# Kernel tuning notes

Measured on AMD Instinct MI355X. Metric: run time of the kernel, lower is better.

Reference implementation:

```python
import jax, jax.numpy as jnp
import numpy as np
from jax import lax

BETA = 0.5        # Sinkhron beta
N_ITER = 20       # got_iteration
THRESH = 0.1      # P > 0.1 threshold
NL_I = 5          # apply_non_linearity(..., 'elu', i=5)
EPS = 1e-9


def setup_inputs() -> dict:
    key = jax.random.key(0)
    k1, k2 = jax.random.split(key)
    B, N, D = 128, 512, 128
    h = jax.random.normal(k1, (B, N, D), dtype=jnp.float32)
    W0 = jnp.ones((D,), dtype=jnp.float32)
    W1 = jnp.ones((D,), dtype=jnp.float32)
    lengths = jax.random.randint(k2, (B,), 0, N, dtype=jnp.int32)
    return {"h": h, "W0": W0, "W1": W1, "lengths": lengths}


def _forward(h, W0, W1, lengths):
    B, N, D = h.shape
    lengths = jnp.maximum(lengths, 1)
    mask = (jnp.arange(N)[None, :] < lengths[:, None])          # [B, N] bool
    mf = mask.astype(h.dtype)
    mask2 = mf[:, :, None] * mf[:, None, :]                      # [B, N, N]

    # internal_forward: Diag layers with relu between (mlp_act='relu')
    h = h * W0
    h = jax.nn.relu(h)
    h = h * W1

    # cost_matrix_batch_torch: cosine similarity, add identity diag, mask
    hn = h / (jnp.linalg.norm(h, axis=-1, keepdims=True) + 1e-12)
    sim = jnp.einsum('bnd,bmd->bnm', hn, hn)                     # [B, N, N]
    sim = sim + jnp.eye(N, dtype=h.dtype)                        # add_eye_diag
    sim = sim * mask2
    cost = (1.0 - sim) * mask2

    # Sinkhorn with uniform marginals on valid nodes, fixed iterations
    n = lengths.astype(h.dtype)
    mu = mf / n[:, None]                                         # [B, N]
    K = jnp.exp(-cost / BETA) * mask2                            # [B, N, N]

    def body(carry, _):
        u, v = carry
        u = mu / (jnp.einsum('bnm,bm->bn', K, v) + EPS) * mf
        v = mu / (jnp.einsum('bnm,bn->bm', K, u) + EPS) * mf
        return (u, v), None

    (u, v), _ = lax.scan(body, (mf, mf), None, length=N_ITER)
    P = u[:, :, None] * K * v[:, None, :]                        # transport plan

    # P.detach(); scale by number of nodes per graph; threshold
    P = lax.stop_gradient(P)
    P = n[:, None, None] * P
    A = (P > THRESH).astype(h.dtype)
    similarity = A * sim
    # apply_non_linearity 'elu': elu(x*i - i) + 1
    out = jax.nn.elu(similarity * NL_I - NL_I) + 1.0
    return out


def reference(h, W0, W1, lengths):
    return _forward(h, W0, W1, lengths)
```

## Files before the change

kernel.cpp:

```cpp
#include <hip/hip_runtime.h>

#define BB 128
#define NN 512
#define DD 128
#define SLOT_STRIDE 544

__global__ __launch_bounds__(256) void hn_kernel(const float* __restrict__ h,
                                                 const float* __restrict__ W0,
                                                 const float* __restrict__ W1,
                                                 float* __restrict__ hn) {
    int wave = (int)((blockIdx.x * blockDim.x + threadIdx.x) >> 6);
    int lane = threadIdx.x & 63;
    const float2* h2 = (const float2*)(h + (size_t)wave * DD);
    float2 w0 = ((const float2*)W0)[lane];
    float2 w1 = ((const float2*)W1)[lane];
    float2 x = h2[lane];
    float p0 = fmaxf(x.x * w0.x, 0.0f) * w1.x;
    float p1 = fmaxf(x.y * w0.y, 0.0f) * w1.y;
    float ss = p0 * p0 + p1 * p1;
#pragma unroll
    for (int m = 32; m; m >>= 1) ss += __shfl_xor(ss, m);
    float inv = 1.0f / (sqrtf(ss) + 1e-12f);
    float2 o;
    o.x = p0 * inv;
    o.y = p1 * inv;
    ((float2*)(hn + (size_t)wave * DD))[lane] = o;
}

#define KC 32
__global__ __launch_bounds__(256) void sim_kernel(const float* __restrict__ hn,
                                                  const int* __restrict__ lengths,
                                                  float* __restrict__ K) {
    __shared__ float As[KC][132];
    __shared__ float Bs[KC][132];
    __shared__ int pre[BB + 1];
    int tid = threadIdx.x;
    if (tid == 0) {
        int acc = 0;
        for (int b = 0; b < BB; b++) {
            pre[b] = acc;
            int len = max(lengths[b], 1);
            int nt = (len + 127) >> 7;
            acc += nt * nt;
        }
        pre[BB] = acc;
    }
    __syncthreads();
    int total = pre[BB];

    int lr = tid >> 3;
    int lk = (tid & 7) << 2;
    int tx = tid & 15, ty = tid >> 4;

    for (int t = blockIdx.x; t < total; t += gridDim.x) {
        int lo = 0, hi = BB;
        while (lo + 1 < hi) {
            int mid = (lo + hi) >> 1;
            if (pre[mid] <= t) lo = mid; else hi = mid;
        }
        int b = lo;
        int local = t - pre[b];
        int len = max(lengths[b], 1);
        int nt = (len + 127) >> 7;
        int ti = local / nt;
        int tj = local - ti * nt;
        int r0 = ti << 7, c0 = tj << 7;
        const float* base = hn + (size_t)b * NN * DD;
        float acc[8][8] = {};

        for (int kc = 0; kc < DD; kc += KC) {
#pragma unroll
            for (int rr = 0; rr < 128; rr += 32) {
                float4 a = *(const float4*)(base + (size_t)(r0 + lr + rr) * DD + kc + lk);
                As[lk + 0][lr + rr] = a.x; As[lk + 1][lr + rr] = a.y;
                As[lk + 2][lr + rr] = a.z; As[lk + 3][lr + rr] = a.w;
                float4 bb = *(const float4*)(base + (size_t)(c0 + lr + rr) * DD + kc + lk);
                Bs[lk + 0][lr + rr] = bb.x; Bs[lk + 1][lr + rr] = bb.y;
                Bs[lk + 2][lr + rr] = bb.z; Bs[lk + 3][lr + rr] = bb.w;
            }
            __syncthreads();
#pragma unroll
            for (int kk = 0; kk < KC; kk++) {
                float4 a0 = *(const float4*)&As[kk][ty * 8];
                float4 a1 = *(const float4*)&As[kk][ty * 8 + 4];
                float4 b0 = *(const float4*)&Bs[kk][tx * 4];
                float4 b1 = *(const float4*)&Bs[kk][64 + tx * 4];
                float ar[8] = {a0.x, a0.y, a0.z, a0.w, a1.x, a1.y, a1.z, a1.w};
                float bc[8] = {b0.x, b0.y, b0.z, b0.w, b1.x, b1.y, b1.z, b1.w};
#pragma unroll
                for (int r = 0; r < 8; r++)
#pragma unroll
                    for (int c = 0; c < 8; c++)
                        acc[r][c] = fmaf(ar[r], bc[c], acc[r][c]);
            }
            __syncthreads();
        }
        float* out = K + (size_t)b * NN * NN;
#pragma unroll
        for (int r = 0; r < 8; r++) {
            int i = r0 + ty * 8 + r;
            if (i >= len) continue;
#pragma unroll
            for (int cg = 0; cg < 2; cg++) {
                int j0 = c0 + cg * 64 + tx * 4;
                if (j0 >= len) continue;
                float vv[4];
#pragma unroll
                for (int c = 0; c < 4; c++) {
                    float s = acc[r][cg * 4 + c] + ((i == j0 + c) ? 1.0f : 0.0f);
                    vv[c] = expf(2.0f * s - 2.0f);
                }
                float4 o;
                o.x = vv[0]; o.y = vv[1]; o.z = vv[2]; o.w = vv[3];
                *(float4*)(out + (size_t)i * NN + j0) = o;
            }
        }
    }
}

__device__ __forceinline__ float dot8(float4 A, float4 B, float4 x0, float4 x1) {
    float d = fmaf(A.x, x0.x, fmaf(A.y, x0.y, fmaf(A.z, x0.z, A.w * x0.w)));
    return fmaf(B.x, x1.x, fmaf(B.y, x1.y, fmaf(B.z, x1.z, fmaf(B.w, x1.w, d))));
}

__global__ __launch_bounds__(512, 4) void coop_sink(const float* __restrict__ K,
                                                    float* __restrict__ u_buf,
                                                    float* __restrict__ v_buf,
                                                    const int* __restrict__ lengths,
                                                    float* __restrict__ slots) {
    __shared__ float xb[NN];
    __shared__ float pv[8 * NN];
    __shared__ int Sh[BB], Pre[BB];

    int g = blockIdx.x;
    int tid = threadIdx.x;

    if (tid == 0) {
        int need[BB]; int ssum = 0;
        for (int m = 0; m < BB; m++) {
            int L = max(lengths[m], 1);
            need[m] = (L + 79) / 80;
            ssum += need[m];
        }
        while (ssum > 512) {
            int best = 0, bv = need[0];
            for (int m = 1; m < BB; m++)
                if (need[m] > bv) { bv = need[m]; best = m; }
            need[best]--; ssum--;
        }
        int acc = 0;
        for (int m = 0; m < BB; m++) { Pre[m] = acc; Sh[m] = need[m]; acc += need[m]; }
    }
    __syncthreads();

    int m = -1;
    for (int mm = 0; mm < BB; mm++)
        if (g >= Pre[mm] && g < Pre[mm] + Sh[mm]) { m = mm; break; }
    if (m < 0) return;
    int b = m;
    int jbase = Pre[m];
    int q = g - jbase;
    int S = Sh[m];

    int len = max(lengths[b], 1);
    int len4 = (len + 3) & ~3;
    int rpq = (len + S - 1) / S;
    int r_lo = q * rpq;
    int nrows = min(len - r_lo, rpq);
    if (nrows < 0) nrows = 0;
    float inv_n = 1.0f / (float)len;

    int w = tid >> 6, l = tid & 63;
    int c0 = 4 * l, c1 = 256 + 4 * l;
    bool a0 = c0 < len4, a1 = c1 < len4;
    const float* Kb = K + (size_t)b * NN * NN;

    xb[tid] = (tid < len) ? 1.0f : 0.0f;

    float4 kA0 = {0,0,0,0}, kA1 = {0,0,0,0}, kA2 = {0,0,0,0}, kA3 = {0,0,0,0};
    float4 kA4 = {0,0,0,0}, kA5 = {0,0,0,0}, kA6 = {0,0,0,0}, kA7 = {0,0,0,0};
    float4 kA8 = {0,0,0,0}, kA9 = {0,0,0,0};
    float4 kB0 = {0,0,0,0}, kB1 = {0,0,0,0}, kB2 = {0,0,0,0}, kB3 = {0,0,0,0};
    float4 kB4 = {0,0,0,0}, kB5 = {0,0,0,0}, kB6 = {0,0,0,0}, kB7 = {0,0,0,0};
    float4 kB8 = {0,0,0,0}, kB9 = {0,0,0,0};
#define FILL_ROW(o)                                                          \
    {                                                                        \
        int i_ = w + 8 * o;                                                  \
        if (i_ < nrows) {                                                    \
            const float* g0_ = Kb + (size_t)(r_lo + i_) * NN;                \
            if (a0) kA##o = *(const float4*)(g0_ + c0);                      \
            if (a1) kB##o = *(const float4*)(g0_ + c1);                      \
        }                                                                    \
    }
    FILL_ROW(0) FILL_ROW(1) FILL_ROW(2) FILL_ROW(3) FILL_ROW(4)
    FILL_ROW(5) FILL_ROW(6) FILL_ROW(7) FILL_ROW(8) FILL_ROW(9)
#undef FILL_ROW

    __syncthreads();

    for (int t = 0; t < 20; t++) {
        float4 xv0 = *(const float4*)(xb + c0);
        float4 xv1 = *(const float4*)(xb + c1);
        float4 pa = {0, 0, 0, 0}, pb = {0, 0, 0, 0};

        float d0 = dot8(kA0, kB0, xv0, xv1);
        float d1 = dot8(kA1, kB1, xv0, xv1);
        float d2 = dot8(kA2, kB2, xv0, xv1);
        float d3 = dot8(kA3, kB3, xv0, xv1);
        float d4 = dot8(kA4, kB4, xv0, xv1);
        float d5 = dot8(kA5, kB5, xv0, xv1);
        float d6 = dot8(kA6, kB6, xv0, xv1);
        float d7 = dot8(kA7, kB7, xv0, xv1);
        float d8 = dot8(kA8, kB8, xv0, xv1);
        float d9 = dot8(kA9, kB9, xv0, xv1);
#pragma unroll
        for (int mm = 32; mm; mm >>= 1) {
            d0 += __shfl_xor(d0, mm); d1 += __shfl_xor(d1, mm);
            d2 += __shfl_xor(d2, mm); d3 += __shfl_xor(d3, mm);
            d4 += __shfl_xor(d4, mm); d5 += __shfl_xor(d5, mm);
            d6 += __shfl_xor(d6, mm); d7 += __shfl_xor(d7, mm);
            d8 += __shfl_xor(d8, mm); d9 += __shfl_xor(d9, mm);
        }
        float u0 = inv_n / (d0 + 1e-9f), u1 = inv_n / (d1 + 1e-9f);
        float u2 = inv_n / (d2 + 1e-9f), u3 = inv_n / (d3 + 1e-9f);
        float u4 = inv_n / (d4 + 1e-9f), u5 = inv_n / (d5 + 1e-9f);
        float u6 = inv_n / (d6 + 1e-9f), u7 = inv_n / (d7 + 1e-9f);
        float u8 = inv_n / (d8 + 1e-9f), u9 = inv_n / (d9 + 1e-9f);
#define ACC_ROW(o, uo)                                                       \
    pa.x = fmaf(kA##o.x, uo, pa.x); pa.y = fmaf(kA##o.y, uo, pa.y);          \
    pa.z = fmaf(kA##o.z, uo, pa.z); pa.w = fmaf(kA##o.w, uo, pa.w);          \
    pb.x = fmaf(kB##o.x, uo, pb.x); pb.y = fmaf(kB##o.y, uo, pb.y);          \
    pb.z = fmaf(kB##o.z, uo, pb.z); pb.w = fmaf(kB##o.w, uo, pb.w);
        ACC_ROW(0, u0) ACC_ROW(1, u1) ACC_ROW(2, u2) ACC_ROW(3, u3)
        ACC_ROW(4, u4) ACC_ROW(5, u5) ACC_ROW(6, u6) ACC_ROW(7, u7)
        ACC_ROW(8, u8) ACC_ROW(9, u9)
#undef ACC_ROW
        if (t == 19 && l == 0) {
            float* ub = u_buf + (size_t)b * NN + r_lo + w;
            if (w + 0 < nrows) ub[0] = u0;
            if (w + 8 < nrows) ub[8] = u1;
            if (w + 16 < nrows) ub[16] = u2;
            if (w + 24 < nrows) ub[24] = u3;
            if (w + 32 < nrows) ub[32] = u4;
            if (w + 40 < nrows) ub[40] = u5;
            if (w + 48 < nrows) ub[48] = u6;
            if (w + 56 < nrows) ub[56] = u7;
            if (w + 64 < nrows) ub[64] = u8;
            if (w + 72 < nrows) ub[72] = u9;
        }

        for (int i = 80 + w; i < nrows; i += 8) {
            const float* g0 = Kb + (size_t)(r_lo + i) * NN;
            float4 A = {0, 0, 0, 0}, B = {0, 0, 0, 0};
            if (a0) A = *(const float4*)(g0 + c0);
            if (a1) B = *(const float4*)(g0 + c1);
            float d = dot8(A, B, xv0, xv1);
#pragma unroll
            for (int mm = 32; mm; mm >>= 1) d += __shfl_xor(d, mm);
            float uu = inv_n / (d + 1e-9f);
            pa.x = fmaf(A.x, uu, pa.x); pa.y = fmaf(A.y, uu, pa.y);
            pa.z = fmaf(A.z, uu, pa.z); pa.w = fmaf(A.w, uu, pa.w);
            pb.x = fmaf(B.x, uu, pb.x); pb.y = fmaf(B.y, uu, pb.y);
            pb.z = fmaf(B.z, uu, pb.z); pb.w = fmaf(B.w, uu, pb.w);
            if (t == 19 && l == 0) u_buf[(size_t)b * NN + r_lo + i] = uu;
        }

        *(float4*)(pv + w * NN + c0) = pa;
        *(float4*)(pv + w * NN + c1) = pb;
        __syncthreads();
        float* slotp = slots + ((size_t)(t & 1) * 512 + g) * SLOT_STRIDE;
        int c = tid;
        float s0 = pv[c] + pv[NN + c] + pv[2 * NN + c] + pv[3 * NN + c] +
                   pv[4 * NN + c] + pv[5 * NN + c] + pv[6 * NN + c] + pv[7 * NN + c];
        __hip_atomic_store(slotp + c, s0, __ATOMIC_RELAXED, __HIP_MEMORY_SCOPE_AGENT);
        asm volatile("s_waitcnt vmcnt(0)" ::: "memory");
        __syncthreads();
        if (tid == 0)
            __hip_atomic_store((int*)(slotp + 512), t + 1, __ATOMIC_RELAXED,
                               __HIP_MEMORY_SCOPE_AGENT);
        if (tid < S && tid != q) {
            const int* tagp = (const int*)(slots +
                ((size_t)(t & 1) * 512 + (size_t)(jbase + tid)) * SLOT_STRIDE + 512);
            while (__hip_atomic_load(tagp, __ATOMIC_RELAXED, __HIP_MEMORY_SCOPE_AGENT) != t + 1)
                __builtin_amdgcn_s_sleep(1);
        }
        __syncthreads();

        const float* sbase = slots + ((size_t)(t & 1) * 512) * SLOT_STRIDE;
        float t0 = s0;
        for (int s = 1; s < S; s++) {
            int k = q + s; if (k >= S) k -= S;
            t0 += __hip_atomic_load(sbase + (size_t)(jbase + k) * SLOT_STRIDE + c,
                                    __ATOMIC_RELAXED, __HIP_MEMORY_SCOPE_AGENT);
        }
        float v0 = (c < len) ? (inv_n / (t0 + 1e-9f)) : 0.0f;
        if (t < 19) {
            xb[c] = v0;
        } else if (c >= r_lo && c < r_lo + nrows) {
            v_buf[(size_t)b * NN + c] = v0;
        }
        __syncthreads();
    }
}

__global__ __launch_bounds__(256) void epi_kernel(float* __restrict__ io,
                                                  const float* __restrict__ u,
                                                  const float* __restrict__ v,
                                                  const int* __restrict__ lengths) {
    const float E5 = 0.006737946999085467f;
    size_t idx = (size_t)blockIdx.x * 256 + threadIdx.x;
    int b = (int)(idx >> 16);
    int r = (int)(idx >> 7) & (NN - 1);
    int c4 = ((int)idx & 127) << 2;
    int len = max(lengths[b], 1);
    float4 o;
    if (r >= len || c4 >= len) {
        o.x = E5; o.y = E5; o.z = E5; o.w = E5;
        ((float4*)io)[idx] = o;
        return;
    }
    float4 k = ((float4*)io)[idx];
    float ui = u[(size_t)b * NN + r];
    float4 vv = *(const float4*)(v + (size_t)b * NN + c4);
    float t = (float)len * ui;
    float kv[4] = {k.x, k.y, k.z, k.w};
    float vj[4] = {vv.x, vv.y, vv.z, vv.w};
    float ov[4];
#pragma unroll
    for (int c = 0; c < 4; c++) {
        float Kc = kv[c];
        float P = t * Kc * vj[c];
        bool valid = (c4 + c) < len;
        if (valid && P > 0.1f) {
            float x = 2.5f * logf(Kc);
            ov[c] = (x > 0.0f) ? (x + 1.0f) : expf(x);
        } else {
            ov[c] = E5;
        }
    }
    o.x = ov[0]; o.y = ov[1]; o.z = ov[2]; o.w = ov[3];
    ((float4*)io)[idx] = o;
}

extern "C" void kernel_launch(void* const* d_in, const int* in_sizes, int n_in,
                              void* d_out, int out_size, void* d_ws, size_t ws_size,
                              hipStream_t stream) {
    const float* h = (const float*)d_in[0];
    const float* W0 = (const float*)d_in[1];
    const float* W1 = (const float*)d_in[2];
    const int* lengths = (const int*)d_in[3];
    float* K = (float*)d_out;

    char* ws = (char*)d_ws;
    float* hn = (float*)ws;
    size_t off = (size_t)BB * NN * DD * 4;
    float* u = (float*)(ws + off);     off += (size_t)BB * NN * 4;
    float* v = (float*)(ws + off);     off += (size_t)BB * NN * 4;
    float* slots = (float*)(ws + off); off += (size_t)2 * 512 * SLOT_STRIDE * 4;

    hn_kernel<<<BB * NN / 4, 256, 0, stream>>>(h, W0, W1, hn);
    sim_kernel<<<1024, 256, 0, stream>>>(hn, lengths, K);

    coop_sink<<<512, 512, 0, stream>>>(K, u, v, lengths, slots);

    epi_kernel<<<(unsigned)((size_t)BB * NN * NN / 4 / 256), 256, 0, stream>>>(K, u, v, lengths);
}
```

Baseline: 393.9 us.

## Cache 176 K rows per block in registers and halve the Sinkhorn grid

Each workgroup now keeps up to 176 rows of K in registers instead of 80, so a graph is split across fewer blocks. The persistent Sinkhorn grid drops from 512 to 256 blocks, and launch bounds allow 2 blocks per CU instead of 4. This cuts cross-block slot exchange and spin-wait synchronisation per iteration, and skips the slot publishing when a graph fits in one block. The cost is much higher register pressure (44 float4 per thread), which risks spills and lower occupancy.

```diff
diff --git a/kernel.cpp b/kernel.cpp
--- a/kernel.cpp
+++ b/kernel.cpp
@@ -123,7 +123,10 @@
     return fmaf(B.x, x1.x, fmaf(B.y, x1.y, fmaf(B.z, x1.z, fmaf(B.w, x1.w, d))));
 }
 
-__global__ __launch_bounds__(512, 4) void coop_sink(const float* __restrict__ K,
+#define ROWS22(X) X(0) X(1) X(2) X(3) X(4) X(5) X(6) X(7) X(8) X(9) X(10) \
+    X(11) X(12) X(13) X(14) X(15) X(16) X(17) X(18) X(19) X(20) X(21)
+
+__global__ __launch_bounds__(512, 2) void coop_sink(const float* __restrict__ K,
                                                     float* __restrict__ u_buf,
                                                     float* __restrict__ v_buf,
                                                     const int* __restrict__ lengths,
@@ -139,10 +142,10 @@
         int need[BB]; int ssum = 0;
         for (int m = 0; m < BB; m++) {
             int L = max(lengths[m], 1);
-            need[m] = (L + 79) / 80;
+            need[m] = (L + 175) / 176;
             ssum += need[m];
         }
-        while (ssum > 512) {
+        while (ssum > 256) {
             int best = 0, bv = need[0];
             for (int m = 1; m < BB; m++)
                 if (need[m] > bv) { bv = need[m]; best = m; }
@@ -177,23 +180,19 @@
 
     xb[tid] = (tid < len) ? 1.0f : 0.0f;
 
-    float4 kA0 = {0,0,0,0}, kA1 = {0,0,0,0}, kA2 = {0,0,0,0}, kA3 = {0,0,0,0};
-    float4 kA4 = {0,0,0,0}, kA5 = {0,0,0,0}, kA6 = {0,0,0,0}, kA7 = {0,0,0,0};
-    float4 kA8 = {0,0,0,0}, kA9 = {0,0,0,0};
-    float4 kB0 = {0,0,0,0}, kB1 = {0,0,0,0}, kB2 = {0,0,0,0}, kB3 = {0,0,0,0};
-    float4 kB4 = {0,0,0,0}, kB5 = {0,0,0,0}, kB6 = {0,0,0,0}, kB7 = {0,0,0,0};
-    float4 kB8 = {0,0,0,0}, kB9 = {0,0,0,0};
+#define DECL(o) float4 kA##o = {0,0,0,0}, kB##o = {0,0,0,0};
+    ROWS22(DECL)
+#undef DECL
 #define FILL_ROW(o)                                                          \
     {                                                                        \
-        int i_ = w + 8 * o;                                                  \
+        int i_ = w + 8 * (o);                                                \
         if (i_ < nrows) {                                                    \
             const float* g0_ = Kb + (size_t)(r_lo + i_) * NN;                \
             if (a0) kA##o = *(const float4*)(g0_ + c0);                      \
             if (a1) kB##o = *(const float4*)(g0_ + c1);                      \
         }                                                                    \
     }
-    FILL_ROW(0) FILL_ROW(1) FILL_ROW(2) FILL_ROW(3) FILL_ROW(4)
-    FILL_ROW(5) FILL_ROW(6) FILL_ROW(7) FILL_ROW(8) FILL_ROW(9)
+    ROWS22(FILL_ROW)
 #undef FILL_ROW
 
     __syncthreads();
@@ -203,53 +202,33 @@
         float4 xv1 = *(const float4*)(xb + c1);
         float4 pa = {0, 0, 0, 0}, pb = {0, 0, 0, 0};
 
-        float d0 = dot8(kA0, kB0, xv0, xv1);
-        float d1 = dot8(kA1, kB1, xv0, xv1);
-        float d2 = dot8(kA2, kB2, xv0, xv1);
-        float d3 = dot8(kA3, kB3, xv0, xv1);
-        float d4 = dot8(kA4, kB4, xv0, xv1);
-        float d5 = dot8(kA5, kB5, xv0, xv1);
-        float d6 = dot8(kA6, kB6, xv0, xv1);
-        float d7 = dot8(kA7, kB7, xv0, xv1);
-        float d8 = dot8(kA8, kB8, xv0, xv1);
-        float d9 = dot8(kA9, kB9, xv0, xv1);
+#define DOT(o) float d##o = dot8(kA##o, kB##o, xv0, xv1);
+        ROWS22(DOT)
+#undef DOT
 #pragma unroll
         for (int mm = 32; mm; mm >>= 1) {
-            d0 += __shfl_xor(d0, mm); d1 += __shfl_xor(d1, mm);
-            d2 += __shfl_xor(d2, mm); d3 += __shfl_xor(d3, mm);
-            d4 += __shfl_xor(d4, mm); d5 += __shfl_xor(d5, mm);
-            d6 += __shfl_xor(d6, mm); d7 += __shfl_xor(d7, mm);
-            d8 += __shfl_xor(d8, mm); d9 += __shfl_xor(d9, mm);
-        }
-        float u0 = inv_n / (d0 + 1e-9f), u1 = inv_n / (d1 + 1e-9f);
-        float u2 = inv_n / (d2 + 1e-9f), u3 = inv_n / (d3 + 1e-9f);
-        float u4 = inv_n / (d4 + 1e-9f), u5 = inv_n / (d5 + 1e-9f);
-        float u6 = inv_n / (d6 + 1e-9f), u7 = inv_n / (d7 + 1e-9f);
-        float u8 = inv_n / (d8 + 1e-9f), u9 = inv_n / (d9 + 1e-9f);
-#define ACC_ROW(o, uo)                                                       \
-    pa.x = fmaf(kA##o.x, uo, pa.x); pa.y = fmaf(kA##o.y, uo, pa.y);          \
-    pa.z = fmaf(kA##o.z, uo, pa.z); pa.w = fmaf(kA##o.w, uo, pa.w);          \
-    pb.x = fmaf(kB##o.x, uo, pb.x); pb.y = fmaf(kB##o.y, uo, pb.y);          \
-    pb.z = fmaf(kB##o.z, uo, pb.z); pb.w = fmaf(kB##o.w, uo, pb.w);
-        ACC_ROW(0, u0) ACC_ROW(1, u1) ACC_ROW(2, u2) ACC_ROW(3, u3)
-        ACC_ROW(4, u4) ACC_ROW(5, u5) ACC_ROW(6, u6) ACC_ROW(7, u7)
-        ACC_ROW(8, u8) ACC_ROW(9, u9)
+#define BF(o) d##o += __shfl_xor(d##o, mm);
+            ROWS22(BF)
+#undef BF
+        }
+#define RC(o) float uu##o = inv_n / (d##o + 1e-9f);
+        ROWS22(RC)
+#undef RC
+#define ACC_ROW(o)                                                           \
+    pa.x = fmaf(kA##o.x, uu##o, pa.x); pa.y = fmaf(kA##o.y, uu##o, pa.y);    \
+    pa.z = fmaf(kA##o.z, uu##o, pa.z); pa.w = fmaf(kA##o.w, uu##o, pa.w);    \
+    pb.x = fmaf(kB##o.x, uu##o, pb.x); pb.y = fmaf(kB##o.y, uu##o, pb.y);    \
+    pb.z = fmaf(kB##o.z, uu##o, pb.z); pb.w = fmaf(kB##o.w, uu##o, pb.w);
+        ROWS22(ACC_ROW)
 #undef ACC_ROW
         if (t == 19 && l == 0) {
             float* ub = u_buf + (size_t)b * NN + r_lo + w;
-            if (w + 0 < nrows) ub[0] = u0;
-            if (w + 8 < nrows) ub[8] = u1;
-            if (w + 16 < nrows) ub[16] = u2;
-            if (w + 24 < nrows) ub[24] = u3;
-            if (w + 32 < nrows) ub[32] = u4;
-            if (w + 40 < nrows) ub[40] = u5;
-            if (w + 48 < nrows) ub[48] = u6;
-            if (w + 56 < nrows) ub[56] = u7;
-            if (w + 64 < nrows) ub[64] = u8;
-            if (w + 72 < nrows) ub[72] = u9;
-        }
-
-        for (int i = 80 + w; i < nrows; i += 8) {
+#define ST(o) if (w + 8 * (o) < nrows) ub[8 * (o)] = uu##o;
+            ROWS22(ST)
+#undef ST
+        }
+
+        for (int i = 176 + w; i < nrows; i += 8) {
             const float* g0 = Kb + (size_t)(r_lo + i) * NN;
             float4 A = {0, 0, 0, 0}, B = {0, 0, 0, 0};
             if (a0) A = *(const float4*)(g0 + c0);
@@ -272,10 +251,12 @@
         int c = tid;
         float s0 = pv[c] + pv[NN + c] + pv[2 * NN + c] + pv[3 * NN + c] +
                    pv[4 * NN + c] + pv[5 * NN + c] + pv[6 * NN + c] + pv[7 * NN + c];
-        __hip_atomic_store(slotp + c, s0, __ATOMIC_RELAXED, __HIP_MEMORY_SCOPE_AGENT);
-        asm volatile("s_waitcnt vmcnt(0)" ::: "memory");
+        if (S > 1) {
+            __hip_atomic_store(slotp + c, s0, __ATOMIC_RELAXED, __HIP_MEMORY_SCOPE_AGENT);
+            asm volatile("s_waitcnt vmcnt(0)" ::: "memory");
+        }
         __syncthreads();
-        if (tid == 0)
+        if (S > 1 && tid == 0)
             __hip_atomic_store((int*)(slotp + 512), t + 1, __ATOMIC_RELAXED,
                                __HIP_MEMORY_SCOPE_AGENT);
         if (tid < S && tid != q) {
@@ -361,7 +342,7 @@
     hn_kernel<<<BB * NN / 4, 256, 0, stream>>>(h, W0, W1, hn);
     sim_kernel<<<1024, 256, 0, stream>>>(hn, lengths, K);
 
-    coop_sink<<<512, 512, 0, stream>>>(K, u, v, lengths, slots);
+    coop_sink<<<256, 512, 0, stream>>>(K, u, v, lengths, slots);
 
     epi_kernel<<<(unsigned)((size_t)BB * NN * NN / 4 / 256), 256, 0, stream>>>(K, u, v, lengths);
 }
```

Measured after the change: 377.8 us. 4.1% less time.
